# Optimization experiments

Hardware: AMD Instinct MI355X
Metric: run time of the kernel (lower is better)

Reference implementation:

```python
import jax, jax.numpy as jnp
import numpy as np

N, C_IN, H, W = 48, 64, 128, 128


def _conv3x3(x, w, b):
    # NCHW conv, kernel 3, stride 1, pad 1 (SAME)
    y = jax.lax.conv_general_dilated(
        x, w, window_strides=(1, 1), padding=((1, 1), (1, 1)),
        dimension_numbers=("NCHW", "OIHW", "NCHW"))
    return y + b[None, :, None, None]


def setup_inputs() -> dict:
    key = jax.random.key(0)
    ks = jax.random.split(key, 4)
    s1 = 1.0 / np.sqrt(C_IN * 9)
    s2 = 1.0 / np.sqrt(128 * 9)
    s3 = 1.0 / np.sqrt(32 * 9)
    return {
        "x": jax.random.normal(ks[0], (N, C_IN, H, W), dtype=jnp.float32),
        "to_process": jnp.arange(N, dtype=jnp.int64) if jax.config.jax_enable_x64 else jnp.arange(N, dtype=jnp.int32),
        "batch_size": 8,
        "W1": jax.random.normal(ks[1], (128, C_IN, 3, 3), dtype=jnp.float32) * s1,
        "b1": jnp.zeros((128,), dtype=jnp.float32),
        "W2": jax.random.normal(ks[2], (32, 128, 3, 3), dtype=jnp.float32) * s2,
        "b2": jnp.zeros((32,), dtype=jnp.float32),
        "W3": jax.random.normal(ks[3], (1, 32, 3, 3), dtype=jnp.float32) * s3,
        "b3": jnp.zeros((1,), dtype=jnp.float32),
    }


def reference(x, to_process, batch_size, W1, b1, W2, b2, W3, b3):
    # x holds only the active sites listed in to_process; all ops are per-site.
    x = jax.nn.relu(_conv3x3(x, W1, b1))          # [N,128,H,W]
    x = jax.nn.relu(_conv3x3(x, W2, b2))          # [N,32,H,W]
    n, c, h, w = x.shape
    # SparseBilinearUpsample(2): half-pixel-center bilinear x2 (align_corners=False)
    x = jax.image.resize(x, (n, c, 2 * h, 2 * w), method="bilinear")
    x = _conv3x3(x, W3, b3)                        # [N,1,2H,2W]
    return x
```

## Files before the change

### kernel.cpp

```cpp
#include <hip/hip_runtime.h>


typedef _Float16 half_t;
typedef _Float16 half2_t __attribute__((ext_vector_type(2)));
typedef _Float16 half4_t __attribute__((ext_vector_type(4)));
typedef _Float16 half8   __attribute__((ext_vector_type(8)));
typedef float    floatx4  __attribute__((ext_vector_type(4)));
typedef float    floatx16 __attribute__((ext_vector_type(16)));

__global__ __launch_bounds__(256) void repack_w(
    const float* __restrict__ W1, const float* __restrict__ W2,
    const float* __restrict__ W3, half_t* __restrict__ wh1,
    half_t* __restrict__ wh2, half_t* __restrict__ wh3)
{
    int idx = blockIdx.x * 256 + threadIdx.x;
    if (idx < 73728) {
        int ci = idx & 63, co = (idx >> 6) & 127, tap = idx >> 13;
        wh1[idx] = (half_t)W1[(co * 64 + ci) * 9 + tap];
    } else if (idx < 110592) {
        int j = idx - 73728;
        int ci = j & 127, co = (j >> 7) & 31, tap = j >> 12;
        wh2[j] = (half_t)W2[(co * 128 + ci) * 9 + tap];
    } else if (idx < 110880) {
        int j = idx - 110592;
        int ci = j & 31, tap = j >> 5;
        wh3[j] = (half_t)W3[ci * 9 + tap];
    }
}

__global__ __launch_bounds__(256) void repack_x(
    const float* __restrict__ x, half_t* __restrict__ xh)
{
    const int tid = threadIdx.x;
    const int px = tid & 127, rr = tid >> 7;
    const int y = blockIdx.x * 2 + rr;
    const int n = blockIdx.y;
    const float* xn = x + (size_t)n * 64 * 16384 + (size_t)y * 128 + px;
    half2_t hb[32];
#pragma unroll
    for (int c2 = 0; c2 < 32; ++c2) {
        float f0 = xn[(size_t)(2 * c2) * 16384];
        float f1 = xn[(size_t)(2 * c2 + 1) * 16384];
        half2_t h; h.x = (half_t)f0; h.y = (half_t)f1;
        hb[c2] = h;
    }
    half_t* op = xh + (((size_t)n * 128 + y) * 128 + px) * 64;
#pragma unroll
    for (int k = 0; k < 8; ++k)
        *(half8*)(op + k * 8) = *(half8*)(&hb[k * 4]);
}

__global__ __launch_bounds__(256, 4) void conv1_mfma(
    const half_t* __restrict__ xh,
    const half_t* __restrict__ wh,
    const float*  __restrict__ bias,
    half_t* __restrict__ y1h)
{
    __shared__ half_t lx[6 * 34 * 72];
    const int tid  = threadIdx.x;
    const int lane = tid & 63;
    const int wave = tid >> 6;
    const int l31 = lane & 31, lq = lane >> 5;
    const int wco = wave >> 1, wpx = wave & 1;
    const int x0 = blockIdx.x * 32, y0 = blockIdx.y * 4;
    const int n = blockIdx.z;
    const half_t* xn = xh + (size_t)n * (128 * 128 * 64);

    for (int idx = tid; idx < 6 * 34 * 8; idx += 256) {
        int ch = idx & 7;
        int col = (idx >> 3) % 34;
        int row = (idx >> 3) / 34;
        int gx = x0 - 1 + col, gy = y0 - 1 + row;
        half8 v = {};
        if ((unsigned)gx < 128u && (unsigned)gy < 128u)
            v = *(const half8*)(xn + ((size_t)gy * 128 + gx) * 64 + ch * 8);
        *(half8*)(&lx[(row * 34 + col) * 72 + ch * 8]) = v;
    }
    __syncthreads();

    floatx16 acc00 = {}, acc01 = {}, acc10 = {}, acc11 = {};

#pragma unroll
    for (int tap = 0; tap < 9; ++tap) {
        const int dy = tap / 3, dx = tap % 3;
        const half_t* wt = wh + tap * (128 * 64) + (wco * 64 + l31) * 64 + lq * 8;
        const half_t* bp = &lx[((wpx * 2 + dy) * 34 + l31 + dx) * 72 + lq * 8];
#pragma unroll
        for (int kc = 0; kc < 4; ++kc) {
            half8 a0 = *(const half8*)(wt + kc * 16);
            half8 a1 = *(const half8*)(wt + 32 * 64 + kc * 16);
            half8 b0 = *(const half8*)(bp + kc * 16);
            half8 b1 = *(const half8*)(bp + 34 * 72 + kc * 16);
            acc00 = __builtin_amdgcn_mfma_f32_32x32x16_f16(a0, b0, acc00, 0, 0, 0);
            acc01 = __builtin_amdgcn_mfma_f32_32x32x16_f16(a0, b1, acc01, 0, 0, 0);
            acc10 = __builtin_amdgcn_mfma_f32_32x32x16_f16(a1, b0, acc10, 0, 0, 0);
            acc11 = __builtin_amdgcn_mfma_f32_32x32x16_f16(a1, b1, acc11, 0, 0, 0);
        }
    }

#pragma unroll
    for (int mf = 0; mf < 2; ++mf) {
        int co0 = wco * 64 + mf * 32 + lq * 4;
#pragma unroll
        for (int nf = 0; nf < 2; ++nf) {
            floatx16 A = (mf == 0) ? (nf == 0 ? acc00 : acc01)
                                   : (nf == 0 ? acc10 : acc11);
            int oy = y0 + wpx * 2 + nf, ox = x0 + l31;
            half_t* op = y1h + (((size_t)n * 128 + oy) * 128 + ox) * 128 + co0;
#pragma unroll
            for (int g = 0; g < 4; ++g) {
                floatx4 bv = *(const floatx4*)(bias + co0 + 8 * g);
                half4_t o;
                o.x = (half_t)fmaxf(A[4 * g + 0] + bv.x, 0.f);
                o.y = (half_t)fmaxf(A[4 * g + 1] + bv.y, 0.f);
                o.z = (half_t)fmaxf(A[4 * g + 2] + bv.z, 0.f);
                o.w = (half_t)fmaxf(A[4 * g + 3] + bv.w, 0.f);
                *(half4_t*)(op + 8 * g) = o;
            }
        }
    }
}

__global__ __launch_bounds__(256, 3) void conv2_mfma(
    const half_t* __restrict__ y1h,
    const half_t* __restrict__ wh,
    const float*  __restrict__ bias,
    half_t* __restrict__ y2h)
{
    __shared__ half_t lx[18 * 18 * 72];
    const int tid  = threadIdx.x;
    const int lane = tid & 63;
    const int wave = tid >> 6;
    const int l15 = lane & 15, quad = lane >> 4;
    const int x0 = blockIdx.x * 16, y0 = blockIdx.y * 16;
    const int n = blockIdx.z;
    const half_t* yn = y1h + (size_t)n * (128 * 128 * 128);

    floatx4 acc[2][4] = {};

    for (int h = 0; h < 2; ++h) {
        for (int idx = tid; idx < 18 * 18 * 8; idx += 256) {
            int ch = idx & 7;
            int col = (idx >> 3) % 18;
            int row = (idx >> 3) / 18;
            int gx = x0 - 1 + col, gy = y0 - 1 + row;
            half8 v = {};
            if ((unsigned)gx < 128u && (unsigned)gy < 128u)
                v = *(const half8*)(yn + ((size_t)gy * 128 + gx) * 128 + h * 64 + ch * 8);
            *(half8*)(&lx[(row * 18 + col) * 72 + ch * 8]) = v;
        }
        __syncthreads();
#pragma unroll
        for (int tap = 0; tap < 9; ++tap) {
            const int dy = tap / 3, dx = tap % 3;
            const half_t* wt = wh + tap * (32 * 128) + l15 * 128 + h * 64 + quad * 8;
#pragma unroll
            for (int kc = 0; kc < 2; ++kc) {
                half8 a0 = *(const half8*)(wt + kc * 32);
                half8 a1 = *(const half8*)(wt + 16 * 128 + kc * 32);
                const half_t* bp = &lx[((wave * 4 + dy) * 18 + l15 + dx) * 72 + kc * 32 + quad * 8];
#pragma unroll
                for (int nf = 0; nf < 4; ++nf) {
                    half8 b = *(const half8*)(bp + nf * (18 * 72));
                    acc[0][nf] = __builtin_amdgcn_mfma_f32_16x16x32_f16(a0, b, acc[0][nf], 0, 0, 0);
                    acc[1][nf] = __builtin_amdgcn_mfma_f32_16x16x32_f16(a1, b, acc[1][nf], 0, 0, 0);
                }
            }
        }
        __syncthreads();
    }

#pragma unroll
    for (int mf = 0; mf < 2; ++mf) {
        int co0 = mf * 16 + quad * 4;
        floatx4 bv = *(const floatx4*)(bias + co0);
#pragma unroll
        for (int nf = 0; nf < 4; ++nf) {
            int oy = y0 + wave * 4 + nf, ox = x0 + l15;
            floatx4 A = acc[mf][nf];
            half4_t o;
            o.x = (half_t)fmaxf(A.x + bv.x, 0.f);
            o.y = (half_t)fmaxf(A.y + bv.y, 0.f);
            o.z = (half_t)fmaxf(A.z + bv.z, 0.f);
            o.w = (half_t)fmaxf(A.w + bv.w, 0.f);
            *(half4_t*)(y2h + (((size_t)n * 128 + oy) * 128 + ox) * 32 + co0) = o;
        }
    }
}

__global__ __launch_bounds__(256) void upsample_k(
    const half_t* __restrict__ y2h, half_t* __restrict__ uh)
{
    int idx = blockIdx.x * 256 + threadIdx.x;
    int X = idx & 255, Y = (idx >> 8) & 255, n = idx >> 16;
    int jx = X >> 1, jy = Y >> 1;
    int jxo = (X & 1) ? (jx < 127 ? jx + 1 : 127) : (jx > 0 ? jx - 1 : 0);
    int jyo = (Y & 1) ? (jy < 127 ? jy + 1 : 127) : (jy > 0 ? jy - 1 : 0);
    const half_t* base = y2h + (size_t)n * (128 * 128 * 32);
    const half_t* p00 = base + ((size_t)jy  * 128 + jx ) * 32;
    const half_t* p01 = base + ((size_t)jy  * 128 + jxo) * 32;
    const half_t* p10 = base + ((size_t)jyo * 128 + jx ) * 32;
    const half_t* p11 = base + ((size_t)jyo * 128 + jxo) * 32;
    half_t* op = uh + (((size_t)n * 256 + Y) * 256 + X) * 32;
#pragma unroll
    for (int c = 0; c < 4; ++c) {
        half8 v00 = *(const half8*)(p00 + c * 8);
        half8 v01 = *(const half8*)(p01 + c * 8);
        half8 v10 = *(const half8*)(p10 + c * 8);
        half8 v11 = *(const half8*)(p11 + c * 8);
        half8 o = v00 * (half_t)0.5625f + (v01 + v10) * (half_t)0.1875f
                + v11 * (half_t)0.0625f;
        *(half8*)(op + c * 8) = o;
    }
}

__global__ __launch_bounds__(256) void conv3_k(
    const half_t* __restrict__ uh,
    const half_t* __restrict__ wh3,
    const float*  __restrict__ bias,
    float* __restrict__ out)
{
    __shared__ half_t lu[10 * 34 * 40];
    const int tid = threadIdx.x;
    const int c = tid & 31, r = tid >> 5;
    const int x0 = blockIdx.x * 32, y0 = blockIdx.y * 8;
    const int n = blockIdx.z;
    const half_t* un = uh + (size_t)n * (256 * 256 * 32);

    for (int idx = tid; idx < 10 * 34 * 4; idx += 256) {
        int ch = idx & 3;
        int col = (idx >> 2) % 34;
        int row = (idx >> 2) / 34;
        int gx = x0 - 1 + col, gy = y0 - 1 + row;
        half8 v = {};
        if ((unsigned)gx < 256u && (unsigned)gy < 256u)
            v = *(const half8*)(un + ((size_t)gy * 256 + gx) * 32 + ch * 8);
        *(half8*)(&lu[(row * 34 + col) * 40 + ch * 8]) = v;
    }
    __syncthreads();

    float acc = 0.f;
#pragma unroll
    for (int tap = 0; tap < 9; ++tap) {
        const int dy = tap / 3, dx = tap % 3;
        const half_t* lp = &lu[((r + dy) * 34 + c + dx) * 40];
        const half_t* wp = wh3 + tap * 32;
#pragma unroll
        for (int cc = 0; cc < 4; ++cc) {
            half8 v = *(const half8*)(lp + cc * 8);
            half8 w = *(const half8*)(wp + cc * 8);
            acc = __builtin_amdgcn_fdot2(__builtin_shufflevector(v, v, 0, 1),
                                         __builtin_shufflevector(w, w, 0, 1), acc, false);
            acc = __builtin_amdgcn_fdot2(__builtin_shufflevector(v, v, 2, 3),
                                         __builtin_shufflevector(w, w, 2, 3), acc, false);
            acc = __builtin_amdgcn_fdot2(__builtin_shufflevector(v, v, 4, 5),
                                         __builtin_shufflevector(w, w, 4, 5), acc, false);
            acc = __builtin_amdgcn_fdot2(__builtin_shufflevector(v, v, 6, 7),
                                         __builtin_shufflevector(w, w, 6, 7), acc, false);
        }
    }
    out[((size_t)n * 256 + (y0 + r)) * 256 + x0 + c] = acc + bias[0];
}

extern "C" void kernel_launch(void* const* d_in, const int* in_sizes, int n_in,
                              void* d_out, int out_size, void* d_ws, size_t ws_size,
                              hipStream_t stream) {
    const float* x  = (const float*)d_in[0];
    const float* W1 = (const float*)d_in[3];
    const float* b1 = (const float*)d_in[4];
    const float* W2 = (const float*)d_in[5];
    const float* b2 = (const float*)d_in[6];
    const float* W3 = (const float*)d_in[7];
    const float* b3 = (const float*)d_in[8];
    float* out = (float*)d_out;

    char* ws = (char*)d_ws;
    half_t* xh  = (half_t*)ws;
    half_t* uh  = (half_t*)ws;
    half_t* y1h = (half_t*)(ws + 201326592ull);
    half_t* y2h = (half_t*)(ws + 402653184ull);
    half_t* wh1 = (half_t*)(ws + 452984832ull);
    half_t* wh2 = wh1 + 73728;
    half_t* wh3 = wh2 + 36864;

    repack_w<<<434, 256, 0, stream>>>(W1, W2, W3, wh1, wh2, wh3);
    repack_x<<<dim3(64, 48), 256, 0, stream>>>(x, xh);
    conv1_mfma<<<dim3(4, 32, 48), 256, 0, stream>>>(xh, wh1, b1, y1h);
    conv2_mfma<<<dim3(8, 8, 48), 256, 0, stream>>>(y1h, wh2, b2, y2h);
    upsample_k<<<12288, 256, 0, stream>>>(y2h, uh);
    conv3_k<<<dim3(8, 32, 48), 256, 0, stream>>>(uh, wh3, b3, out);
}
```

Before: 892.7 us.

## Enlarge conv1 and conv2 output tiles per block for more weight reuse

conv1 now computes 8 output rows per block instead of 4, with each wave holding 2x4 32x32 accumulator fragments, so every weight fragment loaded from global memory feeds twice as many MFMAs. conv2 widens its tile to 32 columns and stages input channels in four 32-channel chunks with a smaller padded LDS stride, doubling its accumulators per wave. The aim is to cut redundant weight loads and halo re-reads per output. In exchange, register pressure and LDS use grow, and conv1's occupancy hint drops from 4 to 2 blocks.

```diff
diff --git a/kernel.cpp b/kernel.cpp
--- a/kernel.cpp
+++ b/kernel.cpp
@@ -50,23 +50,23 @@
         *(half8*)(op + k * 8) = *(half8*)(&hb[k * 4]);
 }
 
-__global__ __launch_bounds__(256, 4) void conv1_mfma(
+__global__ __launch_bounds__(256, 2) void conv1_mfma(
     const half_t* __restrict__ xh,
     const half_t* __restrict__ wh,
     const float*  __restrict__ bias,
     half_t* __restrict__ y1h)
 {
-    __shared__ half_t lx[6 * 34 * 72];
+    __shared__ half_t lx[10 * 34 * 72];
     const int tid  = threadIdx.x;
     const int lane = tid & 63;
     const int wave = tid >> 6;
     const int l31 = lane & 31, lq = lane >> 5;
     const int wco = wave >> 1, wpx = wave & 1;
-    const int x0 = blockIdx.x * 32, y0 = blockIdx.y * 4;
+    const int x0 = blockIdx.x * 32, y0 = blockIdx.y * 8;
     const int n = blockIdx.z;
     const half_t* xn = xh + (size_t)n * (128 * 128 * 64);
 
-    for (int idx = tid; idx < 6 * 34 * 8; idx += 256) {
+    for (int idx = tid; idx < 10 * 34 * 8; idx += 256) {
         int ch = idx & 7;
         int col = (idx >> 3) % 34;
         int row = (idx >> 3) / 34;
@@ -78,23 +78,26 @@
     }
     __syncthreads();
 
-    floatx16 acc00 = {}, acc01 = {}, acc10 = {}, acc11 = {};
+    floatx16 acc[2][4] = {};
 
 #pragma unroll
     for (int tap = 0; tap < 9; ++tap) {
         const int dy = tap / 3, dx = tap % 3;
         const half_t* wt = wh + tap * (128 * 64) + (wco * 64 + l31) * 64 + lq * 8;
-        const half_t* bp = &lx[((wpx * 2 + dy) * 34 + l31 + dx) * 72 + lq * 8];
+        const half_t* bp = &lx[((wpx * 4 + dy) * 34 + l31 + dx) * 72 + lq * 8];
 #pragma unroll
         for (int kc = 0; kc < 4; ++kc) {
             half8 a0 = *(const half8*)(wt + kc * 16);
             half8 a1 = *(const half8*)(wt + 32 * 64 + kc * 16);
-            half8 b0 = *(const half8*)(bp + kc * 16);
-            half8 b1 = *(const half8*)(bp + 34 * 72 + kc * 16);
-            acc00 = __builtin_amdgcn_mfma_f32_32x32x16_f16(a0, b0, acc00, 0, 0, 0);
-            acc01 = __builtin_amdgcn_mfma_f32_32x32x16_f16(a0, b1, acc01, 0, 0, 0);
-            acc10 = __builtin_amdgcn_mfma_f32_32x32x16_f16(a1, b0, acc10, 0, 0, 0);
-            acc11 = __builtin_amdgcn_mfma_f32_32x32x16_f16(a1, b1, acc11, 0, 0, 0);
+            half8 b[4];
+#pragma unroll
+            for (int nf = 0; nf < 4; ++nf)
+                b[nf] = *(const half8*)(bp + nf * (34 * 72) + kc * 16);
+#pragma unroll
+            for (int nf = 0; nf < 4; ++nf) {
+                acc[0][nf] = __builtin_amdgcn_mfma_f32_32x32x16_f16(a0, b[nf], acc[0][nf], 0, 0, 0);
+                acc[1][nf] = __builtin_amdgcn_mfma_f32_32x32x16_f16(a1, b[nf], acc[1][nf], 0, 0, 0);
+            }
         }
     }
 
@@ -102,10 +105,9 @@
     for (int mf = 0; mf < 2; ++mf) {
         int co0 = wco * 64 + mf * 32 + lq * 4;
 #pragma unroll
-        for (int nf = 0; nf < 2; ++nf) {
-            floatx16 A = (mf == 0) ? (nf == 0 ? acc00 : acc01)
-                                   : (nf == 0 ? acc10 : acc11);
-            int oy = y0 + wpx * 2 + nf, ox = x0 + l31;
+        for (int nf = 0; nf < 4; ++nf) {
+            floatx16 A = acc[mf][nf];
+            int oy = y0 + wpx * 4 + nf, ox = x0 + l31;
             half_t* op = y1h + (((size_t)n * 128 + oy) * 128 + ox) * 128 + co0;
 #pragma unroll
             for (int g = 0; g < 4; ++g) {
@@ -127,44 +129,42 @@
     const float*  __restrict__ bias,
     half_t* __restrict__ y2h)
 {
-    __shared__ half_t lx[18 * 18 * 72];
+    __shared__ half_t lx[18 * 34 * 40];
     const int tid  = threadIdx.x;
     const int lane = tid & 63;
-    const int wave = tid >> 6;
+    const int w    = tid >> 6;
     const int l15 = lane & 15, quad = lane >> 4;
-    const int x0 = blockIdx.x * 16, y0 = blockIdx.y * 16;
+    const int x0 = blockIdx.x * 32, y0 = blockIdx.y * 16;
     const int n = blockIdx.z;
     const half_t* yn = y1h + (size_t)n * (128 * 128 * 128);
 
-    floatx4 acc[2][4] = {};
-
-    for (int h = 0; h < 2; ++h) {
-        for (int idx = tid; idx < 18 * 18 * 8; idx += 256) {
-            int ch = idx & 7;
-            int col = (idx >> 3) % 18;
-            int row = (idx >> 3) / 18;
+    floatx4 acc[2][8] = {};
+
+    for (int h = 0; h < 4; ++h) {
+        for (int idx = tid; idx < 18 * 34 * 4; idx += 256) {
+            int ch = idx & 3;
+            int col = (idx >> 2) % 34;
+            int row = (idx >> 2) / 34;
             int gx = x0 - 1 + col, gy = y0 - 1 + row;
             half8 v = {};
             if ((unsigned)gx < 128u && (unsigned)gy < 128u)
-                v = *(const half8*)(yn + ((size_t)gy * 128 + gx) * 128 + h * 64 + ch * 8);
-            *(half8*)(&lx[(row * 18 + col) * 72 + ch * 8]) = v;
+                v = *(const half8*)(yn + ((size_t)gy * 128 + gx) * 128 + h * 32 + ch * 8);
+            *(half8*)(&lx[(row * 34 + col) * 40 + ch * 8]) = v;
         }
         __syncthreads();
 #pragma unroll
         for (int tap = 0; tap < 9; ++tap) {
             const int dy = tap / 3, dx = tap % 3;
-            const half_t* wt = wh + tap * (32 * 128) + l15 * 128 + h * 64 + quad * 8;
-#pragma unroll
-            for (int kc = 0; kc < 2; ++kc) {
-                half8 a0 = *(const half8*)(wt + kc * 32);
-                half8 a1 = *(const half8*)(wt + 16 * 128 + kc * 32);
-                const half_t* bp = &lx[((wave * 4 + dy) * 18 + l15 + dx) * 72 + kc * 32 + quad * 8];
-#pragma unroll
-                for (int nf = 0; nf < 4; ++nf) {
-                    half8 b = *(const half8*)(bp + nf * (18 * 72));
-                    acc[0][nf] = __builtin_amdgcn_mfma_f32_16x16x32_f16(a0, b, acc[0][nf], 0, 0, 0);
-                    acc[1][nf] = __builtin_amdgcn_mfma_f32_16x16x32_f16(a1, b, acc[1][nf], 0, 0, 0);
-                }
+            const half_t* wt = wh + tap * (32 * 128) + l15 * 128 + h * 32 + quad * 8;
+            half8 a0 = *(const half8*)(wt);
+            half8 a1 = *(const half8*)(wt + 16 * 128);
+#pragma unroll
+            for (int nf = 0; nf < 8; ++nf) {
+                int rr = w * 4 + (nf >> 1) + dy;
+                int cc = (nf & 1) * 16 + l15 + dx;
+                half8 b = *(const half8*)(&lx[(rr * 34 + cc) * 40 + quad * 8]);
+                acc[0][nf] = __builtin_amdgcn_mfma_f32_16x16x32_f16(a0, b, acc[0][nf], 0, 0, 0);
+                acc[1][nf] = __builtin_amdgcn_mfma_f32_16x16x32_f16(a1, b, acc[1][nf], 0, 0, 0);
             }
         }
         __syncthreads();
@@ -175,8 +175,8 @@
         int co0 = mf * 16 + quad * 4;
         floatx4 bv = *(const floatx4*)(bias + co0);
 #pragma unroll
-        for (int nf = 0; nf < 4; ++nf) {
-            int oy = y0 + wave * 4 + nf, ox = x0 + l15;
+        for (int nf = 0; nf < 8; ++nf) {
+            int oy = y0 + w * 4 + (nf >> 1), ox = x0 + (nf & 1) * 16 + l15;
             floatx4 A = acc[mf][nf];
             half4_t o;
             o.x = (half_t)fmaxf(A.x + bv.x, 0.f);
@@ -285,8 +285,8 @@
 
     repack_w<<<434, 256, 0, stream>>>(W1, W2, W3, wh1, wh2, wh3);
     repack_x<<<dim3(64, 48), 256, 0, stream>>>(x, xh);
-    conv1_mfma<<<dim3(4, 32, 48), 256, 0, stream>>>(xh, wh1, b1, y1h);
-    conv2_mfma<<<dim3(8, 8, 48), 256, 0, stream>>>(y1h, wh2, b2, y2h);
+    conv1_mfma<<<dim3(4, 16, 48), 256, 0, stream>>>(xh, wh1, b1, y1h);
+    conv2_mfma<<<dim3(4, 8, 48), 256, 0, stream>>>(y1h, wh2, b2, y2h);
     upsample_k<<<12288, 256, 0, stream>>>(y2h, uh);
     conv3_k<<<dim3(8, 32, 48), 256, 0, stream>>>(uh, wh3, b3, out);
 }
```

Result: faster. 832.2 us (-6.8%).
